# Kernel tuning notes

Hardware: AMD Instinct MI355X
Metric: run time of the kernel (lower is better)

## Reference

```python
import jax, jax.numpy as jnp
import numpy as np
from jax import lax

KS = 3
PAD = 1
N = KS * KS


def setup_inputs() -> dict:
    key = jax.random.key(0)
    k1, k2, k3, k4, k5, k6 = jax.random.split(key, 6)
    b, cin, cout, h, w = 4, 64, 64, 256, 256
    x = jax.random.normal(k1, (b, cin, h, w), jnp.float32)
    # offset-predicting conv: 2*N output channels, 3x3, pad 1
    p_conv_w = 0.1 * jax.random.normal(k2, (2 * N, cin, KS, KS), jnp.float32)
    p_conv_b = jnp.zeros((2 * N,), jnp.float32)
    # main conv applied to the k*k-expanded sampled map (no bias in original)
    conv_w = jax.random.normal(k3, (cout, cin, KS, KS), jnp.float32) / np.sqrt(cin * N)
    bn_gamma = 1.0 + 0.1 * jax.random.normal(k4, (cout,), jnp.float32)
    bn_beta = 0.1 * jax.random.normal(k5, (cout,), jnp.float32)
    return {"x": x, "p_conv_w": p_conv_w, "p_conv_b": p_conv_b,
            "conv_w": conv_w, "bn_gamma": bn_gamma, "bn_beta": bn_beta}


def _deform_conv(x, p_conv_w, p_conv_b, conv_w, bn_gamma, bn_beta):
    b, c, h, w = x.shape
    # offsets: (b, 2N, h, w) -> (b, h, w, 2N)
    offset = lax.conv_general_dilated(x, p_conv_w, (1, 1), ((PAD, PAD), (PAD, PAD)))
    offset = offset + p_conv_b[None, :, None, None]
    offset = jnp.transpose(offset, (0, 2, 3, 1))
    # zero-pad input; sampling coordinates live on the padded grid
    x_pad = jnp.pad(x, ((0, 0), (0, 0), (PAD, PAD), (PAD, PAD)))
    Hp, Wp = h + 2 * PAD, w + 2 * PAD
    # p = p_0 + p_n + offset  (x/y coords each of shape (b,h,w,N))
    r = jnp.arange(-(KS - 1) // 2, KS // 2 + 1, dtype=jnp.float32)  # [-1,0,1]
    pn_x, pn_y = jnp.meshgrid(r, r, indexing="ij")
    pn_x, pn_y = pn_x.reshape(-1), pn_y.reshape(-1)  # (N,)
    p0_x = jnp.arange(1, h + 1, dtype=jnp.float32)[:, None, None]  # (h,1,1)
    p0_y = jnp.arange(1, w + 1, dtype=jnp.float32)[None, :, None]  # (1,w,1)
    p_x = offset[..., :N] + p0_x + pn_x  # (b,h,w,N)
    p_y = offset[..., N:] + p0_y + pn_y
    # integer corner coords (detached / non-differentiable), clamped
    fx = jnp.floor(lax.stop_gradient(p_x))
    fy = jnp.floor(lax.stop_gradient(p_y))
    q_lt_x = jnp.clip(fx, 0, Hp - 1).astype(jnp.int32)
    q_lt_y = jnp.clip(fy, 0, Wp - 1).astype(jnp.int32)
    q_rb_x = jnp.clip(fx + 1, 0, Hp - 1).astype(jnp.int32)
    q_rb_y = jnp.clip(fy + 1, 0, Wp - 1).astype(jnp.int32)
    # clamped continuous coords (gradient flows to offsets)
    px = jnp.clip(p_x, 0, Hp - 1)
    py = jnp.clip(p_y, 0, Wp - 1)
    # bilinear weights
    ltx = q_lt_x.astype(px.dtype); lty = q_lt_y.astype(px.dtype)
    rbx = q_rb_x.astype(px.dtype); rby = q_rb_y.astype(px.dtype)
    g_lt = (1 + (ltx - px)) * (1 + (lty - py))
    g_rb = (1 - (rbx - px)) * (1 - (rby - py))
    g_lb = (1 + (ltx - px)) * (1 - (rby - py))
    g_rt = (1 - (rbx - px)) * (1 + (lty - py))
    x_flat = x_pad.reshape(b, c, Hp * Wp)

    def gather(qx, qy):
        idx = (qx * Wp + qy).reshape(b, 1, -1)  # (b,1,h*w*N)
        out = jnp.take_along_axis(x_flat, idx, axis=2)
        return out.reshape(b, c, h, w, N)

    x_off = (g_lt[:, None] * gather(q_lt_x, q_lt_y)
             + g_rb[:, None] * gather(q_rb_x, q_rb_y)
             + g_lb[:, None] * gather(q_lt_x, q_rb_y)
             + g_rt[:, None] * gather(q_rb_x, q_lt_y))  # (b,c,h,w,N)
    # conv (kernel=KS, stride=KS on k*k-expanded map) == contraction over (c,N)
    out = jnp.einsum("bchwn,ocn->bohw", x_off, conv_w.reshape(conv_w.shape[0], c, N))
    # BatchNorm2d (training-mode batch statistics) + LeakyReLU(0.1)
    mean = out.mean(axis=(0, 2, 3), keepdims=True)
    var = out.var(axis=(0, 2, 3), keepdims=True)
    y = (out - mean) * lax.rsqrt(var + 1e-5)
    y = y * bn_gamma[None, :, None, None] + bn_beta[None, :, None, None]
    return jnp.where(y > 0, y, 0.1 * y)


def reference(x, p_conv_w, p_conv_b, conv_w, bn_gamma, bn_beta):
    return _deform_conv(x, p_conv_w, p_conv_b, conv_w, bn_gamma, bn_beta)
```

## Files before the change

### kernel.cpp

```cpp
#include <hip/hip_runtime.h>
#include <math.h>

#define BB 4
#define CC 64
#define OCC 64
#define HH 256
#define WW 256
#define HP 258
#define WP 258
#define NPIX (BB * HH * WW)
#define CNT_F 262144.0f

typedef __attribute__((ext_vector_type(8))) __bf16 bf16x8;
typedef __attribute__((ext_vector_type(4))) float f32x4;

__device__ __forceinline__ float blo(unsigned u) {
    return __builtin_bit_cast(float, u << 16);
}
__device__ __forceinline__ float bhi(unsigned u) {
    return __builtin_bit_cast(float, u & 0xffff0000u);
}

__global__ __launch_bounds__(256) void pad_transpose(const float* __restrict__ x,
                                                     __bf16* __restrict__ xt) {
    int blk = blockIdx.x;
    int xchunk = blk & 3;
    int y = (blk >> 2) & 255;
    int b = blk >> 10;
    int tid = threadIdx.x;
    __shared__ float tile[64][65];
    int x0 = xchunk * 64;
    int col = tid & 63;
    int crow = tid >> 6;
    const float* xp = x + ((size_t)b * CC) * HH * WW + (size_t)y * WW + x0;
#pragma unroll
    for (int i = 0; i < 16; ++i) {
        int c = crow + i * 4;
        tile[c][col] = xp[(size_t)c * HH * WW + col];
    }
    __syncthreads();
    __bf16* op = xt + (((size_t)b * HP + (y + 1)) * WP + (x0 + 1)) * CC;
#pragma unroll
    for (int i = 0; i < 16; ++i) {
        int xl = crow + i * 4;
        op[(size_t)xl * CC + col] = (__bf16)tile[col][xl];
    }
}

__global__ void zero_border(__bf16* __restrict__ xt) {
    int i = blockIdx.x * 256 + threadIdx.x;
    const int total = BB * 1028 * CC;
    if (i >= total) return;
    int c = i & 63;
    int p = (i >> 6) % 1028;
    int b = (i >> 6) / 1028;
    int yp, xp;
    if (p < 258)      { yp = 0;           xp = p; }
    else if (p < 516) { yp = 257;         xp = p - 258; }
    else if (p < 772) { yp = p - 516 + 1; xp = 0; }
    else              { yp = p - 772 + 1; xp = 257; }
    xt[(((size_t)b * HP + yp) * WP + xp) * CC + c] = (__bf16)0.0f;
}

__global__ void reorder_weights(const float* __restrict__ cw,
                                const float* __restrict__ pw,
                                __bf16* __restrict__ wtb,
                                __bf16* __restrict__ pwb) {
    int i = blockIdx.x * 256 + threadIdx.x;
    if (i < 36864) {
        int c = i & 63;
        int n = (i >> 6) % 9;
        int oc = i / 576;
        wtb[i] = (__bf16)cw[((size_t)oc * CC + c) * 9 + n];
    } else {
        int j = i - 36864;
        if (j >= 18432) return;
        int c = j & 63;
        int n = (j >> 6) % 9;
        int oc = j / 576;
        pwb[j] = (__bf16)(oc < 18 ? pw[((size_t)oc * CC + c) * 9 + n] : 0.0f);
    }
}

__global__ __launch_bounds__(256, 8) void offset_strip(const __bf16* __restrict__ xt,
                                                       const __bf16* __restrict__ pwb,
                                                       const float* __restrict__ pb,
                                                       float* __restrict__ off) {
    int phys = blockIdx.x;
    int blk = (phys & 7) * 1024 + (phys >> 3);
    int xq = blk & 7;
    int y  = (blk >> 3) & 255;
    int b  = blk >> 11;
    int x0 = xq * 32;
    int tid = threadIdx.x;
    int wave = tid >> 6, lane = tid & 63;

    __shared__ __attribute__((aligned(16))) __bf16 sS[3][34][72];

    {
        const char* base = (const char*)xt + (size_t)b * HP * WP * CC * 2;
        for (int t = tid; t < 3264; t += 256) {
            int pos = t >> 5, cp = t & 31;
            int r = pos / 34, j = pos - r * 34;
            unsigned d = *(const unsigned*)(base
                + (size_t)((y + r) * WP + (x0 + j)) * (CC * 2) + cp * 4);
            *(unsigned*)&sS[r][j][cp * 2] = d;
        }
    }
    __syncthreads();

    int mh = wave & 1, nh = wave >> 1;
    int m = lane & 15, q = lane >> 4;
    int p_a = mh * 16 + m;
    f32x4 acc = {0.0f, 0.0f, 0.0f, 0.0f};
    const __bf16* bp = pwb + (size_t)(nh * 16 + m) * 576 + q * 8;
#pragma unroll
    for (int n = 0; n < 9; ++n) {
        int dy = n / 3, dx = n - dy * 3;
        const __bf16* abase = &sS[dy][p_a + dx][q * 8];
#pragma unroll
        for (int h = 0; h < 2; ++h) {
            bf16x8 a  = *(const bf16x8*)(abase + h * 32);
            bf16x8 bv = *(const bf16x8*)(bp + n * 64 + h * 32);
            acc = __builtin_amdgcn_mfma_f32_16x16x32_bf16(a, bv, acc, 0, 0, 0);
        }
    }
    int oc = nh * 16 + m;
    if (oc < 18) {
        float bias = pb[oc];
        float* ob = off + (((size_t)(b * 18 + oc)) * HH + y) * WW + x0 + mh * 16 + q * 4;
        float4 v;
        v.x = acc[0] + bias;
        v.y = acc[1] + bias;
        v.z = acc[2] + bias;
        v.w = acc[3] + bias;
        *(float4*)ob = v;
    }
}

__global__ __launch_bounds__(256, 8) void deform_mfma16(const __bf16* __restrict__ xt,
                                                        const float* __restrict__ off,
                                                        const __bf16* __restrict__ wtb,
                                                        float* __restrict__ out) {
    int phys = blockIdx.x;
    int blk = (phys & 7) * 2048 + (phys >> 3);
    int xh = blk & 15;
    int y  = (blk >> 4) & 255;
    int b  = blk >> 12;
    int x0 = xh * 16;
    int tid = threadIdx.x;
    int wave = tid >> 6, lane = tid & 63;
    int chp = lane & 31, half = lane >> 5;

    __shared__ __attribute__((aligned(16))) __bf16 sA[16][576];

    float g0 = 0.0f, g1 = 0.0f, g2 = 0.0f, g3 = 0.0f;
    int c0 = 0, c1 = 0, c2 = 0, c3 = 0;
    if (lane < 36) {
        int t = wave * 36 + lane;
        int n = t >> 4, p = t & 15;
        float offx = off[(((size_t)(b * 18 + n)) * HH + y) * WW + x0 + p];
        float offy = off[(((size_t)(b * 18 + n + 9)) * HH + y) * WW + x0 + p];
        float px = offx + (float)(y + 1) + (float)(n / 3 - 1);
        float py = offy + (float)(x0 + p + 1) + (float)(n % 3 - 1);
        float fx = floorf(px), fy = floorf(py);
        float pxc = fminf(fmaxf(px, 0.0f), 257.0f);
        float pyc = fminf(fmaxf(py, 0.0f), 257.0f);
        int ltx = (int)fminf(fmaxf(fx, 0.0f), 257.0f);
        int lty = (int)fminf(fmaxf(fy, 0.0f), 257.0f);
        int rbx = (int)fminf(fmaxf(fx + 1.0f, 0.0f), 257.0f);
        int rby = (int)fminf(fmaxf(fy + 1.0f, 0.0f), 257.0f);
        float dxl = 1.0f + ((float)ltx - pxc);
        float dxr = 1.0f - ((float)rbx - pxc);
        float dyl = 1.0f + ((float)lty - pyc);
        float dyr = 1.0f - ((float)rby - pyc);
        g0 = dxl * dyl;
        g1 = dxr * dyr;
        g2 = dxl * dyr;
        g3 = dxr * dyl;
        c0 = ((ltx * WP + lty) * CC) * 2;
        c1 = ((rbx * WP + rby) * CC) * 2;
        c2 = ((ltx * WP + rby) * CC) * 2;
        c3 = ((rbx * WP + lty) * CC) * 2;
    }

    {
        const char* xbl = (const char*)xt + (size_t)b * HP * WP * CC * 2 + (size_t)chp * 4;
        char* sAb = (char*)sA;
#pragma unroll 3
        for (int r = 0; r < 18; ++r) {
            int src = r * 2 + half;
            float gx = __shfl(g0, src, 64);
            float gy = __shfl(g1, src, 64);
            float gz = __shfl(g2, src, 64);
            float gw = __shfl(g3, src, 64);
            int vx = __shfl(c0, src, 64);
            int vy = __shfl(c1, src, 64);
            int vz = __shfl(c2, src, 64);
            int vw = __shfl(c3, src, 64);
            unsigned d0 = *(const unsigned*)(xbl + vx);
            unsigned d1 = *(const unsigned*)(xbl + vy);
            unsigned d2 = *(const unsigned*)(xbl + vz);
            unsigned d3 = *(const unsigned*)(xbl + vw);
            float lo = gx * blo(d0) + gy * blo(d1) + gz * blo(d2) + gw * blo(d3);
            float hi = gx * bhi(d0) + gy * bhi(d1) + gz * bhi(d2) + gw * bhi(d3);
            __bf16 rlo = (__bf16)lo, rhi = (__bf16)hi;
            ushort2 rv;
            rv.x = __builtin_bit_cast(unsigned short, rlo);
            rv.y = __builtin_bit_cast(unsigned short, rhi);
            int t = wave * 36 + src;
            int n = t >> 4, p = t & 15;
            unsigned bo = (unsigned)p * 1152u + (unsigned)n * 128u + (unsigned)chp * 4u;
            bo ^= (unsigned)((p & 7) << 4);
            *(ushort2*)(sAb + bo) = rv;
        }
    }
    __syncthreads();

    int m = lane & 15, q = lane >> 4;
    f32x4 acc = {0.0f, 0.0f, 0.0f, 0.0f};
    {
        const char* sAb = (const char*)sA;
        unsigned rowb = (unsigned)m * 1152u;
        unsigned key = (unsigned)((m & 7) << 4);
        const __bf16* bp = wtb + (size_t)(wave * 16 + m) * 576 + q * 8;
        __builtin_amdgcn_s_setprio(1);
#pragma unroll
        for (int k0 = 0; k0 < 576; k0 += 32) {
            unsigned bo = rowb + (((unsigned)(k0 * 2 + q * 16)) ^ key);
            bf16x8 a  = *(const bf16x8*)(sAb + bo);
            bf16x8 bv = *(const bf16x8*)(bp + k0);
            acc = __builtin_amdgcn_mfma_f32_16x16x32_bf16(a, bv, acc, 0, 0, 0);
        }
        __builtin_amdgcn_s_setprio(0);
    }

    int oc = wave * 16 + m;
    float* ob = out + (((size_t)b * OCC + oc) * HH + y) * WW + x0 + q * 4;
    float4 v;
    v.x = acc[0]; v.y = acc[1]; v.z = acc[2]; v.w = acc[3];
    *(float4*)ob = v;
}

__global__ __launch_bounds__(256) void stats_kernel(const float* __restrict__ out,
                                                    float* __restrict__ stats) {
    int blk = blockIdx.x;
    int b = blk & 3;
    int oc = blk >> 2;
    const float* p = out + ((size_t)b * OCC + oc) * HH * WW;
    float s = 0.0f, q = 0.0f;
    for (int i = threadIdx.x; i < HH * WW; i += 256) {
        float v = p[i];
        s += v;
        q += v * v;
    }
#pragma unroll
    for (int d = 1; d < 64; d <<= 1) {
        s += __shfl_xor(s, d, 64);
        q += __shfl_xor(q, d, 64);
    }
    __shared__ float sm[8];
    int wave = threadIdx.x >> 6, lane = threadIdx.x & 63;
    if (lane == 0) { sm[wave] = s; sm[4 + wave] = q; }
    __syncthreads();
    if (threadIdx.x == 0) {
        float ts = sm[0] + sm[1] + sm[2] + sm[3];
        float tq = sm[4] + sm[5] + sm[6] + sm[7];
        atomicAdd(&stats[oc], ts);
        atomicAdd(&stats[64 + oc], tq);
    }
}

__global__ __launch_bounds__(256) void bn_leaky(float* __restrict__ out,
                                                const float* __restrict__ stats,
                                                const float* __restrict__ gamma,
                                                const float* __restrict__ beta) {
    int i = blockIdx.x * 256 + threadIdx.x;
    int oc = (i >> 14) & 63;
    float mean = stats[oc] * (1.0f / CNT_F);
    float var = stats[64 + oc] * (1.0f / CNT_F) - mean * mean;
    float scale = gamma[oc] * rsqrtf(var + 1e-5f);
    float shift = beta[oc] - mean * scale;
    float4* o4 = (float4*)out;
    float4 v = o4[i];
    v.x = v.x * scale + shift; v.x = v.x > 0.0f ? v.x : 0.1f * v.x;
    v.y = v.y * scale + shift; v.y = v.y > 0.0f ? v.y : 0.1f * v.y;
    v.z = v.z * scale + shift; v.z = v.z > 0.0f ? v.z : 0.1f * v.z;
    v.w = v.w * scale + shift; v.w = v.w > 0.0f ? v.w : 0.1f * v.w;
    o4[i] = v;
}

extern "C" void kernel_launch(void* const* d_in, const int* in_sizes, int n_in,
                              void* d_out, int out_size, void* d_ws, size_t ws_size,
                              hipStream_t stream) {
    (void)in_sizes; (void)n_in; (void)out_size; (void)ws_size;
    const float* x     = (const float*)d_in[0];
    const float* pw    = (const float*)d_in[1];
    const float* pb    = (const float*)d_in[2];
    const float* cw    = (const float*)d_in[3];
    const float* gamma = (const float*)d_in[4];
    const float* beta  = (const float*)d_in[5];
    float* out = (float*)d_out;
    char* ws = (char*)d_ws;

    __bf16* xtb  = (__bf16*)ws;
    float*  off  = (float*)(ws + 34080768);
    __bf16* wtb  = (__bf16*)(ws + 34080768 + 18874368);
    __bf16* pwb  = (__bf16*)(ws + 34080768 + 18874368 + 73728);
    float*  stats = (float*)(ws + 34080768 + 18874368 + 73728 + 36864);

    hipMemsetAsync(stats, 0, 128 * sizeof(float), stream);
    pad_transpose<<<4096, 256, 0, stream>>>(x, xtb);
    zero_border<<<(BB * 1028 * CC + 255) / 256, 256, 0, stream>>>(xtb);
    reorder_weights<<<216, 256, 0, stream>>>(cw, pw, wtb, pwb);
    offset_strip<<<8192, 256, 0, stream>>>(xtb, pwb, pb, off);
    deform_mfma16<<<16384, 256, 0, stream>>>(xtb, off, wtb, out);
    stats_kernel<<<OCC * BB, 256, 0, stream>>>(out, stats);
    bn_leaky<<<NPIX * OCC / 4 / 256, 256, 0, stream>>>(out, stats, gamma, beta);
}
```

Measured before the change: 451.7 us.

## Fuse offset convolution into deformable sampling kernel via shared memory

Measured after the change: 438.8 us. 2.9% less time.

```diff
diff --git a/kernel.cpp b/kernel.cpp
--- a/kernel.cpp
+++ b/kernel.cpp
@@ -82,66 +82,11 @@
     }
 }
 
-__global__ __launch_bounds__(256, 8) void offset_strip(const __bf16* __restrict__ xt,
+__global__ __launch_bounds__(256, 8) void deform_fused(const __bf16* __restrict__ xt,
                                                        const __bf16* __restrict__ pwb,
                                                        const float* __restrict__ pb,
-                                                       float* __restrict__ off) {
-    int phys = blockIdx.x;
-    int blk = (phys & 7) * 1024 + (phys >> 3);
-    int xq = blk & 7;
-    int y  = (blk >> 3) & 255;
-    int b  = blk >> 11;
-    int x0 = xq * 32;
-    int tid = threadIdx.x;
-    int wave = tid >> 6, lane = tid & 63;
-
-    __shared__ __attribute__((aligned(16))) __bf16 sS[3][34][72];
-
-    {
-        const char* base = (const char*)xt + (size_t)b * HP * WP * CC * 2;
-        for (int t = tid; t < 3264; t += 256) {
-            int pos = t >> 5, cp = t & 31;
-            int r = pos / 34, j = pos - r * 34;
-            unsigned d = *(const unsigned*)(base
-                + (size_t)((y + r) * WP + (x0 + j)) * (CC * 2) + cp * 4);
-            *(unsigned*)&sS[r][j][cp * 2] = d;
-        }
-    }
-    __syncthreads();
-
-    int mh = wave & 1, nh = wave >> 1;
-    int m = lane & 15, q = lane >> 4;
-    int p_a = mh * 16 + m;
-    f32x4 acc = {0.0f, 0.0f, 0.0f, 0.0f};
-    const __bf16* bp = pwb + (size_t)(nh * 16 + m) * 576 + q * 8;
-#pragma unroll
-    for (int n = 0; n < 9; ++n) {
-        int dy = n / 3, dx = n - dy * 3;
-        const __bf16* abase = &sS[dy][p_a + dx][q * 8];
-#pragma unroll
-        for (int h = 0; h < 2; ++h) {
-            bf16x8 a  = *(const bf16x8*)(abase + h * 32);
-            bf16x8 bv = *(const bf16x8*)(bp + n * 64 + h * 32);
-            acc = __builtin_amdgcn_mfma_f32_16x16x32_bf16(a, bv, acc, 0, 0, 0);
-        }
-    }
-    int oc = nh * 16 + m;
-    if (oc < 18) {
-        float bias = pb[oc];
-        float* ob = off + (((size_t)(b * 18 + oc)) * HH + y) * WW + x0 + mh * 16 + q * 4;
-        float4 v;
-        v.x = acc[0] + bias;
-        v.y = acc[1] + bias;
-        v.z = acc[2] + bias;
-        v.w = acc[3] + bias;
-        *(float4*)ob = v;
-    }
-}
-
-__global__ __launch_bounds__(256, 8) void deform_mfma16(const __bf16* __restrict__ xt,
-                                                        const float* __restrict__ off,
-                                                        const __bf16* __restrict__ wtb,
-                                                        float* __restrict__ out) {
+                                                       const __bf16* __restrict__ wtb,
+                                                       float* __restrict__ out) {
     int phys = blockIdx.x;
     int blk = (phys & 7) * 2048 + (phys >> 3);
     int xh = blk & 15;
@@ -152,15 +97,56 @@
     int wave = tid >> 6, lane = tid & 63;
     int chp = lane & 31, half = lane >> 5;
 
-    __shared__ __attribute__((aligned(16))) __bf16 sA[16][576];
+    __shared__ __attribute__((aligned(16))) char smem[19584];
+    __bf16 (*sS)[18][72] = (__bf16 (*)[18][72])smem;
+    char* sAb = smem;
+    float* offbuf = (float*)(smem + 18432);
+
+    {
+        const char* base = (const char*)xt + (size_t)b * HP * WP * CC * 2;
+        for (int t = tid; t < 1728; t += 256) {
+            int pos = t >> 5, cp = t & 31;
+            int r = pos / 18, j = pos - r * 18;
+            unsigned d = *(const unsigned*)(base
+                + (size_t)((y + r) * WP + (x0 + j)) * (CC * 2) + cp * 4);
+            *(unsigned*)&sS[r][j][cp * 2] = d;
+        }
+    }
+    __syncthreads();
+
+    if (wave < 2) {
+        int nh = wave;
+        int m = lane & 15, q = lane >> 4;
+        f32x4 acc = {0.0f, 0.0f, 0.0f, 0.0f};
+        const __bf16* bp = pwb + (size_t)(nh * 16 + m) * 576 + q * 8;
+#pragma unroll
+        for (int n = 0; n < 9; ++n) {
+            int dy = n / 3, dx = n - dy * 3;
+            const __bf16* abase = &sS[dy][m + dx][q * 8];
+#pragma unroll
+            for (int h = 0; h < 2; ++h) {
+                bf16x8 a  = *(const bf16x8*)(abase + h * 32);
+                bf16x8 bv = *(const bf16x8*)(bp + n * 64 + h * 32);
+                acc = __builtin_amdgcn_mfma_f32_16x16x32_bf16(a, bv, acc, 0, 0, 0);
+            }
+        }
+        int oc = nh * 16 + m;
+        if (oc < 18) {
+            float bias = pb[oc];
+#pragma unroll
+            for (int r = 0; r < 4; ++r)
+                offbuf[(q * 4 + r) * 18 + oc] = acc[r] + bias;
+        }
+    }
+    __syncthreads();
 
     float g0 = 0.0f, g1 = 0.0f, g2 = 0.0f, g3 = 0.0f;
     int c0 = 0, c1 = 0, c2 = 0, c3 = 0;
     if (lane < 36) {
         int t = wave * 36 + lane;
         int n = t >> 4, p = t & 15;
-        float offx = off[(((size_t)(b * 18 + n)) * HH + y) * WW + x0 + p];
-        float offy = off[(((size_t)(b * 18 + n + 9)) * HH + y) * WW + x0 + p];
+        float offx = offbuf[p * 18 + n];
+        float offy = offbuf[p * 18 + n + 9];
         float px = offx + (float)(y + 1) + (float)(n / 3 - 1);
         float py = offy + (float)(x0 + p + 1) + (float)(n % 3 - 1);
         float fx = floorf(px), fy = floorf(py);
@@ -186,7 +172,6 @@
 
     {
         const char* xbl = (const char*)xt + (size_t)b * HP * WP * CC * 2 + (size_t)chp * 4;
-        char* sAb = (char*)sA;
 #pragma unroll 3
         for (int r = 0; r < 18; ++r) {
             int src = r * 2 + half;
@@ -220,7 +205,6 @@
     int m = lane & 15, q = lane >> 4;
     f32x4 acc = {0.0f, 0.0f, 0.0f, 0.0f};
     {
-        const char* sAb = (const char*)sA;
         unsigned rowb = (unsigned)m * 1152u;
         unsigned key = (unsigned)((m & 7) << 4);
         const __bf16* bp = wtb + (size_t)(wave * 16 + m) * 576 + q * 8;
@@ -304,7 +288,6 @@
     char* ws = (char*)d_ws;
 
     __bf16* xtb  = (__bf16*)ws;
-    float*  off  = (float*)(ws + 34080768);
     __bf16* wtb  = (__bf16*)(ws + 34080768 + 18874368);
     __bf16* pwb  = (__bf16*)(ws + 34080768 + 18874368 + 73728);
     float*  stats = (float*)(ws + 34080768 + 18874368 + 73728 + 36864);
@@ -313,8 +296,7 @@
     pad_transpose<<<4096, 256, 0, stream>>>(x, xtb);
     zero_border<<<(BB * 1028 * CC + 255) / 256, 256, 0, stream>>>(xtb);
     reorder_weights<<<216, 256, 0, stream>>>(cw, pw, wtb, pwb);
-    offset_strip<<<8192, 256, 0, stream>>>(xtb, pwb, pb, off);
-    deform_mfma16<<<16384, 256, 0, stream>>>(xtb, off, wtb, out);
+    deform_fused<<<16384, 256, 0, stream>>>(xtb, pwb, pb, wtb, out);
     stats_kernel<<<OCC * BB, 256, 0, stream>>>(out, stats);
     bn_leaky<<<NPIX * OCC / 4 / 256, 256, 0, stream>>>(out, stats, gamma, beta);
 }
```
